# Kernel optimization log

Hardware: AMD Instinct MI355X
Metric: run time of the kernel (lower is better)

The kernel has to match this reference:

```python
import jax, jax.numpy as jnp
import numpy as np

N = 50000
E = 800000
IN_C = 128
HID = 64
HEADS = 4
OUT_C = 1
NEG_SLOPE = 0.2  # PyG GATConv default


def setup_inputs() -> dict:
    key = jax.random.key(0)
    ks = jax.random.split(key, 12)
    s = 1.0 / np.sqrt(IN_C)
    s2 = 1.0 / np.sqrt(HEADS * HID)
    return {
        "x": jax.random.normal(ks[0], (N, IN_C), jnp.float32),
        "edge_index": jax.random.randint(ks[1], (2, E), 0, N, jnp.int64),
        # layer 1 params (heads=HEADS, concat=True)
        "W1": jax.random.normal(ks[2], (IN_C, HEADS * HID), jnp.float32) * s,
        "att_src1": jax.random.normal(ks[3], (HEADS, HID), jnp.float32) * s,
        "att_dst1": jax.random.normal(ks[4], (HEADS, HID), jnp.float32) * s,
        "b1": jnp.zeros((HEADS * HID,), jnp.float32),
        # layer 2 params (heads=1, concat=False)
        "W2": jax.random.normal(ks[5], (HEADS * HID, OUT_C), jnp.float32) * s2,
        "att_src2": jax.random.normal(ks[6], (1, OUT_C), jnp.float32) * s2,
        "att_dst2": jax.random.normal(ks[7], (1, OUT_C), jnp.float32) * s2,
        "b2": jnp.zeros((OUT_C,), jnp.float32),
    }


def _gat_layer(x, src, dst, W, att_src, att_dst, b, concat):
    heads, out_c = att_src.shape
    h = (x @ W).reshape(-1, heads, out_c)          # [N, H, F]
    # per-node attention scores, gathered per edge (scalars, cheap)
    s_src = jnp.einsum('nhf,hf->nh', h, att_src)   # [N, H]
    s_dst = jnp.einsum('nhf,hf->nh', h, att_dst)
    e = jax.nn.leaky_relu(s_src[src] + s_dst[dst], NEG_SLOPE)  # [E, H]
    # segment softmax over edges sharing a destination
    m = jax.ops.segment_max(e, dst, num_segments=N)            # [N, H]
    m = jnp.where(jnp.isfinite(m), m, 0.0)
    ex = jnp.exp(e - m[dst])
    denom = jax.ops.segment_sum(ex, dst, num_segments=N)       # [N, H]
    alpha = ex / denom[dst]                                    # [E, H]
    # weighted scatter-aggregate of source features
    agg = jax.ops.segment_sum(alpha[:, :, None] * h[src], dst, num_segments=N)  # [N, H, F]
    out = agg.reshape(-1, heads * out_c) if concat else agg.mean(axis=1)
    return out + b


def reference(x, edge_index, W1, att_src1, att_dst1, b1, W2, att_src2, att_dst2, b2):
    # PyG GATConv default: add self loops
    loop = jnp.arange(N, dtype=edge_index.dtype)
    src = jnp.concatenate([edge_index[0], loop])
    dst = jnp.concatenate([edge_index[1], loop])
    h = _gat_layer(x, src, dst, W1, att_src1, att_dst1, b1, concat=True)
    h = jax.nn.elu(h)
    return _gat_layer(h, src, dst, W2, att_src2, att_dst2, b2, concat=False)
```

## Files before the change

### kernel.cpp

```cpp
#include <hip/hip_runtime.h>
#include <math.h>

#define NN 50000
#define EE 800000
#define ETOT 850000
#define NEG 0.2f
#define CAP 64
#define NBLK 782
#define NSLC 6250
#define FGRP 256
#define NFB (FGRP * 8)
#define CHK2 1661
#define FITER 7
#define CBLK 3321

typedef unsigned short ushort_t;
typedef __attribute__((ext_vector_type(8))) short bf16x8;
typedef __attribute__((ext_vector_type(4))) float f32x4;

__device__ __forceinline__ unsigned f2bf(float f) {
    unsigned u = __float_as_uint(f);
    return (u + 0x7FFFu + ((u >> 16) & 1u)) >> 16;
}
__device__ __forceinline__ unsigned cvtpk(float lo, float hi) {
    unsigned r;
    asm("v_cvt_pk_bf16_f32 %0, %1, %2" : "=v"(r) : "v"(lo), "v"(hi));
    return r;
}
__device__ __forceinline__ float blo(unsigned u) { return __uint_as_float(u << 16); }
__device__ __forceinline__ float bhi(unsigned u) { return __uint_as_float(u & 0xffff0000u); }

__global__ __launch_bounds__(256) void k_prep(const float* __restrict__ W,
                                              const float* __restrict__ b1,
                                              const float* __restrict__ W2,
                                              const void* ei,
                                              ushort_t* __restrict__ Wf,
                                              float* __restrict__ b1q,
                                              float* __restrict__ W2q,
                                              int* __restrict__ cursor,
                                              ushort_t* __restrict__ dst16,
                                              ushort_t* __restrict__ src16) {
    int bid = blockIdx.x, t = threadIdx.x;
    if (bid < 128) {
        int idx = bid * 256 + t;
        int e = idx & 7, l = (idx >> 3) & 63, ct = (idx >> 9) & 15, kt = idx >> 13;
        int k = kt * 32 + (l >> 4) * 8 + e;
        int col = ct * 16 + (l & 15);
        Wf[idx] = (ushort_t)f2bf(W[k * 256 + col]);
        return;
    }
    if (bid == 128) {
        if (t < 64) {
            int c = t;
            int hl = c >> 1, sub = c & 1, head = c >> 4, lrr = c & 15;
#pragma unroll
            for (int kk = 0; kk < 4; ++kk) {
                b1q[hl * 8 + sub * 4 + kk] = b1[head * 64 + lrr + 16 * kk];
                W2q[hl * 8 + sub * 4 + kk] = W2[head * 64 + lrr + 16 * kk];
            }
        }
        return;
    }
    if (bid < 178) {
        int idx = (bid - 129) * 256 + t;
        if (idx < NN / 4) ((int4*)cursor)[idx] = make_int4(0, 0, 0, 0);
        return;
    }
    int lane = t & 63;
    long long probe = ((const long long*)ei)[lane];
    unsigned long long bad = __ballot(probe < 0 || probe >= NN);
    bool f64 = (bad == 0ull);
    int e = (bid - 178) * 256 + t;
    if (e >= ETOT) return;
    int src, dst;
    if (e < EE) {
        if (f64) {
            src = (int)((const long long*)ei)[e];
            dst = (int)((const long long*)ei)[(long long)EE + e];
        } else {
            src = ((const int*)ei)[e];
            dst = ((const int*)ei)[EE + e];
        }
    } else {
        src = dst = e - EE;
    }
    dst16[e] = (ushort_t)dst;
    src16[e] = (ushort_t)src;
}

__global__ __launch_bounds__(256) void k_main(
    const float* __restrict__ x, const ushort_t* __restrict__ Wf,
    const float* __restrict__ aS, const float* __restrict__ aD,
    const ushort_t* __restrict__ dst16, const ushort_t* __restrict__ src16,
    int* cursor, ushort_t* __restrict__ esrc,
    uint2* __restrict__ h1c, float* __restrict__ sS, float* __restrict__ sD) {
    __shared__ ushort_t xs[64][144];
    int bid = blockIdx.x, t = threadIdx.x;
    if (bid >= NBLK) {
        int s = bid & 7;
        int g = (bid - NBLK) >> 3;
        int lo = s * NSLC;
#pragma unroll
        for (int it = 0; it < FITER; ++it) {
            int c = g + it * FGRP;
            if (c >= CHK2) break;
            int eA = c * 512 + t;
            int eB = eA + 256;
            bool vA = eA < ETOT, vB = eB < ETOT;
            int dstA = 0, dstB = 0;
            if (vA) dstA = dst16[eA];
            if (vB) dstB = dst16[eB];
            if (vA && (unsigned)(dstA - lo) < (unsigned)NSLC) {
                int src = src16[eA];
                int pos = atomicAdd(&cursor[dstA], 1);
                if (pos < CAP) esrc[dstA * CAP + pos] = (ushort_t)src;
            }
            if (vB && (unsigned)(dstB - lo) < (unsigned)NSLC) {
                int src = src16[eB];
                int pos = atomicAdd(&cursor[dstB], 1);
                if (pos < CAP) esrc[dstB * CAP + pos] = (ushort_t)src;
            }
        }
        return;
    }
    int wid = t >> 6, l = t & 63;
    int lg = l >> 4, lr = l & 15;
    int r0 = bid * 64;
    int c0 = wid * 64;
    for (int i = t; i < 1024; i += 256) {
        int row = i >> 4, c = i & 15;
        int gr = r0 + row;
        if (gr >= NN) gr = NN - 1;
        const f32x4* p = (const f32x4*)(x + (size_t)gr * 128 + c * 8);
        f32x4 a = __builtin_nontemporal_load(p);
        f32x4 b = __builtin_nontemporal_load(p + 1);
        uint4 v;
        v.x = cvtpk(a.x, a.y);
        v.y = cvtpk(a.z, a.w);
        v.z = cvtpk(b.x, b.y);
        v.w = cvtpk(b.z, b.w);
        *(uint4*)&xs[row][c * 8] = v;
    }
    __syncthreads();
    const bf16x8* Bv = (const bf16x8*)Wf;
    f32x4 acc[4][4] = {};
#pragma unroll
    for (int kt = 0; kt < 4; ++kt) {
        bf16x8 a[4];
#pragma unroll
        for (int rt = 0; rt < 4; ++rt)
            a[rt] = *(const bf16x8*)&xs[rt * 16 + lr][kt * 32 + lg * 8];
#pragma unroll
        for (int ct = 0; ct < 4; ++ct) {
            bf16x8 b = Bv[(size_t)((kt * 16 + wid * 4 + ct) * 64 + l)];
#pragma unroll
            for (int rt = 0; rt < 4; ++rt)
                acc[rt][ct] = __builtin_amdgcn_mfma_f32_16x16x32_bf16(a[rt], b, acc[rt][ct], 0, 0, 0);
        }
    }
    float aSl[4], aDl[4];
#pragma unroll
    for (int ct = 0; ct < 4; ++ct) {
        aSl[ct] = aS[c0 + ct * 16 + lr];
        aDl[ct] = aD[c0 + ct * 16 + lr];
    }
#pragma unroll
    for (int rt = 0; rt < 4; ++rt) {
#pragma unroll
        for (int q = 0; q < 4; ++q) {
            int row = r0 + rt * 16 + lg * 4 + q;
            bool ok = row < NN;
            float v0 = acc[rt][0][q], v1 = acc[rt][1][q];
            float v2 = acc[rt][2][q], v3 = acc[rt][3][q];
            float p = v0 * aSl[0] + v1 * aSl[1] + v2 * aSl[2] + v3 * aSl[3];
            float dd = v0 * aDl[0] + v1 * aDl[1] + v2 * aDl[2] + v3 * aDl[3];
            uint2 u;
            u.x = cvtpk(v0, v1);
            u.y = cvtpk(v2, v3);
            if (ok) h1c[(size_t)row * 64 + wid * 16 + lr] = u;
#pragma unroll
            for (int k = 8; k >= 1; k >>= 1) {
                p += __shfl_xor(p, k, 64);
                dd += __shfl_xor(dd, k, 64);
            }
            if (ok && lr == 0) {
                sS[row * 4 + wid] = p;
                sD[row * 4 + wid] = dd;
            }
        }
    }
}

__global__ __launch_bounds__(256) void k_agg1(
    const int* __restrict__ cursor, const ushort_t* __restrict__ esrc,
    const uint4* __restrict__ h1c4, const float* __restrict__ sS,
    const float* __restrict__ sD, const float* __restrict__ b1q,
    const float* __restrict__ W2q, float* __restrict__ g) {
    __shared__ float al_lds[4][CAP][4];
    __shared__ int s_lds[4][CAP];
    int wid = threadIdx.x >> 6, lane = threadIdx.x & 63;
    int n = blockIdx.x * 4 + wid;
    if (n >= NN) return;
    int d = cursor[n];
    if (d > CAP) d = CAP;
    int dp = (d + 7) & ~7;
    float4 sd = *(const float4*)(sD + (size_t)n * 4);
    float e0 = -1e30f, e1 = -1e30f, e2 = -1e30f, e3 = -1e30f;
    int s = 0;
    if (lane < d) {
        s = esrc[n * CAP + lane];
        float4 ss = *(const float4*)(sS + (size_t)s * 4);
        e0 = ss.x + sd.x; e0 = e0 > 0.f ? e0 : NEG * e0;
        e1 = ss.y + sd.y; e1 = e1 > 0.f ? e1 : NEG * e1;
        e2 = ss.z + sd.z; e2 = e2 > 0.f ? e2 : NEG * e2;
        e3 = ss.w + sd.w; e3 = e3 > 0.f ? e3 : NEG * e3;
    }
    float m0 = e0, m1 = e1, m2 = e2, m3 = e3;
#pragma unroll
    for (int k = 32; k >= 1; k >>= 1) {
        m0 = fmaxf(m0, __shfl_xor(m0, k, 64));
        m1 = fmaxf(m1, __shfl_xor(m1, k, 64));
        m2 = fmaxf(m2, __shfl_xor(m2, k, 64));
        m3 = fmaxf(m3, __shfl_xor(m3, k, 64));
    }
    float x0 = __expf(e0 - m0);
    float x1 = __expf(e1 - m1);
    float x2 = __expf(e2 - m2);
    float x3 = __expf(e3 - m3);
    float q0 = x0, q1 = x1, q2 = x2, q3 = x3;
#pragma unroll
    for (int k = 32; k >= 1; k >>= 1) {
        q0 += __shfl_xor(q0, k, 64);
        q1 += __shfl_xor(q1, k, 64);
        q2 += __shfl_xor(q2, k, 64);
        q3 += __shfl_xor(q3, k, 64);
    }
    if (lane < dp) {
        al_lds[wid][lane][0] = x0 / q0;
        al_lds[wid][lane][1] = x1 / q1;
        al_lds[wid][lane][2] = x2 / q2;
        al_lds[wid][lane][3] = x3 / q3;
        s_lds[wid][lane] = s;
    }
    __builtin_amdgcn_s_barrier();
    int hl = lane & 31, p = lane >> 5;
    int head = hl >> 3;
    float a0 = 0.f, a1 = 0.f, a2 = 0.f, a3 = 0.f;
    float a4 = 0.f, a5 = 0.f, a6 = 0.f, a7 = 0.f;
    for (int j = 0; j < dp; j += 8) {
        int i0 = j + p, i1 = j + 2 + p, i2 = j + 4 + p, i3 = j + 6 + p;
        int s0 = s_lds[wid][i0];
        int s1 = s_lds[wid][i1];
        int s2 = s_lds[wid][i2];
        int s3 = s_lds[wid][i3];
        float w0 = al_lds[wid][i0][head];
        float w1 = al_lds[wid][i1][head];
        float w2 = al_lds[wid][i2][head];
        float w3 = al_lds[wid][i3][head];
        uint4 u0 = h1c4[(size_t)s0 * 32 + hl];
        uint4 u1 = h1c4[(size_t)s1 * 32 + hl];
        uint4 u2 = h1c4[(size_t)s2 * 32 + hl];
        uint4 u3 = h1c4[(size_t)s3 * 32 + hl];
        a0 = fmaf(w0, blo(u0.x), a0); a1 = fmaf(w0, bhi(u0.x), a1);
        a2 = fmaf(w0, blo(u0.y), a2); a3 = fmaf(w0, bhi(u0.y), a3);
        a4 = fmaf(w0, blo(u0.z), a4); a5 = fmaf(w0, bhi(u0.z), a5);
        a6 = fmaf(w0, blo(u0.w), a6); a7 = fmaf(w0, bhi(u0.w), a7);
        a0 = fmaf(w1, blo(u1.x), a0); a1 = fmaf(w1, bhi(u1.x), a1);
        a2 = fmaf(w1, blo(u1.y), a2); a3 = fmaf(w1, bhi(u1.y), a3);
        a4 = fmaf(w1, blo(u1.z), a4); a5 = fmaf(w1, bhi(u1.z), a5);
        a6 = fmaf(w1, blo(u1.w), a6); a7 = fmaf(w1, bhi(u1.w), a7);
        a0 = fmaf(w2, blo(u2.x), a0); a1 = fmaf(w2, bhi(u2.x), a1);
        a2 = fmaf(w2, blo(u2.y), a2); a3 = fmaf(w2, bhi(u2.y), a3);
        a4 = fmaf(w2, blo(u2.z), a4); a5 = fmaf(w2, bhi(u2.z), a5);
        a6 = fmaf(w2, blo(u2.w), a6); a7 = fmaf(w2, bhi(u2.w), a7);
        a0 = fmaf(w3, blo(u3.x), a0); a1 = fmaf(w3, bhi(u3.x), a1);
        a2 = fmaf(w3, blo(u3.y), a2); a3 = fmaf(w3, bhi(u3.y), a3);
        a4 = fmaf(w3, blo(u3.z), a4); a5 = fmaf(w3, bhi(u3.z), a5);
        a6 = fmaf(w3, blo(u3.w), a6); a7 = fmaf(w3, bhi(u3.w), a7);
    }
    a0 += __shfl_xor(a0, 32, 64); a1 += __shfl_xor(a1, 32, 64);
    a2 += __shfl_xor(a2, 32, 64); a3 += __shfl_xor(a3, 32, 64);
    a4 += __shfl_xor(a4, 32, 64); a5 += __shfl_xor(a5, 32, 64);
    a6 += __shfl_xor(a6, 32, 64); a7 += __shfl_xor(a7, 32, 64);
    float4 bA = ((const float4*)b1q)[hl * 2];
    float4 bB = ((const float4*)b1q)[hl * 2 + 1];
    float4 wA = ((const float4*)W2q)[hl * 2];
    float4 wB = ((const float4*)W2q)[hl * 2 + 1];
    float o0 = a0 + bA.x, o1 = a1 + bA.y, o2 = a2 + bA.z, o3 = a3 + bA.w;
    float o4 = a4 + bB.x, o5 = a5 + bB.y, o6 = a6 + bB.z, o7 = a7 + bB.w;
    o0 = o0 > 0.f ? o0 : expm1f(o0);
    o1 = o1 > 0.f ? o1 : expm1f(o1);
    o2 = o2 > 0.f ? o2 : expm1f(o2);
    o3 = o3 > 0.f ? o3 : expm1f(o3);
    o4 = o4 > 0.f ? o4 : expm1f(o4);
    o5 = o5 > 0.f ? o5 : expm1f(o5);
    o6 = o6 > 0.f ? o6 : expm1f(o6);
    o7 = o7 > 0.f ? o7 : expm1f(o7);
    float part = o0 * wA.x + o1 * wA.y + o2 * wA.z + o3 * wA.w
               + o4 * wB.x + o5 * wB.y + o6 * wB.z + o7 * wB.w;
#pragma unroll
    for (int k = 16; k >= 1; k >>= 1) part += __shfl_xor(part, k, 64);
    if (lane == 0) g[n] = part;
}

__global__ __launch_bounds__(256) void k_layer2(
    const int* __restrict__ cursor, const ushort_t* __restrict__ esrc,
    const float* __restrict__ g, const float* __restrict__ aS2,
    const float* __restrict__ aD2, const float* __restrict__ b2,
    float* __restrict__ out) {
    int wid = threadIdx.x >> 6, lane = threadIdx.x & 63;
    int n = blockIdx.x * 4 + wid;
    if (n >= NN) return;
    int d = cursor[n];
    if (d > CAP) d = CAP;
    float aS = aS2[0], aD = aD2[0];
    float dn = g[n] * aD;
    float gv = 0.f, e = -1e30f;
    if (lane < d) {
        gv = g[esrc[n * CAP + lane]];
        e = gv * aS + dn;
        e = e > 0.f ? e : NEG * e;
    }
    float m = e;
#pragma unroll
    for (int k = 32; k >= 1; k >>= 1) m = fmaxf(m, __shfl_xor(m, k, 64));
    float ex = (lane < d) ? __expf(e - m) : 0.f;
    float den = ex, ws = ex * gv;
#pragma unroll
    for (int k = 32; k >= 1; k >>= 1) {
        den += __shfl_xor(den, k, 64);
        ws += __shfl_xor(ws, k, 64);
    }
    if (lane == 0) out[n] = ws / den + b2[0];
}

extern "C" void kernel_launch(void* const* d_in, const int* in_sizes, int n_in,
                              void* d_out, int out_size, void* d_ws, size_t ws_size,
                              hipStream_t stream) {
    const float* x   = (const float*)d_in[0];
    const void*  ei  = d_in[1];
    const float* W1  = (const float*)d_in[2];
    const float* aS1 = (const float*)d_in[3];
    const float* aD1 = (const float*)d_in[4];
    const float* b1  = (const float*)d_in[5];
    const float* W2  = (const float*)d_in[6];
    const float* aS2 = (const float*)d_in[7];
    const float* aD2 = (const float*)d_in[8];
    const float* b2  = (const float*)d_in[9];
    float* out = (float*)d_out;

    char* w = (char*)d_ws;
    size_t off = 0;
    auto take = [&](size_t bytes) {
        char* p = w + off;
        off = (off + bytes + 255) & ~(size_t)255;
        return p;
    };
    int*      cursor = (int*)take((size_t)NN * 4);
    ushort_t* esrc   = (ushort_t*)take((size_t)NN * CAP * 2);
    ushort_t* dst16  = (ushort_t*)take((size_t)ETOT * 2);
    ushort_t* src16  = (ushort_t*)take((size_t)ETOT * 2);
    float*    sS     = (float*)take((size_t)NN * 4 * 4);
    float*    sD     = (float*)take((size_t)NN * 4 * 4);
    float*    g      = (float*)take((size_t)NN * 4);
    void*     h1c    = take((size_t)NN * 64 * 8);
    ushort_t* Wf     = (ushort_t*)take((size_t)128 * 256 * 2);
    float*    b1q    = (float*)take((size_t)256 * 4);
    float*    W2q    = (float*)take((size_t)256 * 4);
    (void)ws_size; (void)in_sizes; (void)n_in; (void)out_size;

    k_prep<<<178 + CBLK, 256, 0, stream>>>(W1, b1, W2, ei, Wf, b1q, W2q,
                                           cursor, dst16, src16);
    k_main<<<NBLK + NFB, 256, 0, stream>>>(x, Wf, aS1, aD1, dst16, src16,
                                           cursor, esrc, (uint2*)h1c, sS, sD);
    k_agg1<<<12500, 256, 0, stream>>>(cursor, esrc, (const uint4*)h1c, sS, sD, b1q, W2q, g);
    k_layer2<<<12500, 256, 0, stream>>>(cursor, esrc, g, aS2, aD2, b2, out);
}
```

Baseline: 142.8 us.

## Vectorize edge bucketing loads and split layer-1 aggregation into two launches

The bucketing blocks in k_main now load 8 consecutive dst/src indices per thread with 128-bit loads, replacing the strided two-edge-per-iteration loop. FGRP grows so each block covers 2048 edges in a single pass. Separately, k_agg1 takes a base node offset and is launched twice over halves of the nodes, which adds a launch while changing how blocks are scheduled. Atomics per thread are now serialized in 8-element runs, which may lower memory-level parallelism.

```diff
diff --git a/kernel.cpp b/kernel.cpp
--- a/kernel.cpp
+++ b/kernel.cpp
@@ -8,10 +8,8 @@
 #define CAP 64
 #define NBLK 782
 #define NSLC 6250
-#define FGRP 256
+#define FGRP 416
 #define NFB (FGRP * 8)
-#define CHK2 1661
-#define FITER 7
 #define CBLK 3321
 
 typedef unsigned short ushort_t;
@@ -98,27 +96,36 @@
     int bid = blockIdx.x, t = threadIdx.x;
     if (bid >= NBLK) {
         int s = bid & 7;
-        int g = (bid - NBLK) >> 3;
+        int grp = (bid - NBLK) >> 3;
         int lo = s * NSLC;
-#pragma unroll
-        for (int it = 0; it < FITER; ++it) {
-            int c = g + it * FGRP;
-            if (c >= CHK2) break;
-            int eA = c * 512 + t;
-            int eB = eA + 256;
-            bool vA = eA < ETOT, vB = eB < ETOT;
-            int dstA = 0, dstB = 0;
-            if (vA) dstA = dst16[eA];
-            if (vB) dstB = dst16[eB];
-            if (vA && (unsigned)(dstA - lo) < (unsigned)NSLC) {
-                int src = src16[eA];
-                int pos = atomicAdd(&cursor[dstA], 1);
-                if (pos < CAP) esrc[dstA * CAP + pos] = (ushort_t)src;
-            }
-            if (vB && (unsigned)(dstB - lo) < (unsigned)NSLC) {
-                int src = src16[eB];
-                int pos = atomicAdd(&cursor[dstB], 1);
-                if (pos < CAP) esrc[dstB * CAP + pos] = (ushort_t)src;
+        int e0 = grp * 2048 + t * 8;
+        if (e0 >= ETOT) return;
+        ushort_t d[8], sv[8];
+        if (e0 + 8 <= ETOT) {
+            uint4 dv = *(const uint4*)(dst16 + e0);
+            uint4 vv = *(const uint4*)(src16 + e0);
+            d[0] = (ushort_t)dv.x; d[1] = (ushort_t)(dv.x >> 16);
+            d[2] = (ushort_t)dv.y; d[3] = (ushort_t)(dv.y >> 16);
+            d[4] = (ushort_t)dv.z; d[5] = (ushort_t)(dv.z >> 16);
+            d[6] = (ushort_t)dv.w; d[7] = (ushort_t)(dv.w >> 16);
+            sv[0] = (ushort_t)vv.x; sv[1] = (ushort_t)(vv.x >> 16);
+            sv[2] = (ushort_t)vv.y; sv[3] = (ushort_t)(vv.y >> 16);
+            sv[4] = (ushort_t)vv.z; sv[5] = (ushort_t)(vv.z >> 16);
+            sv[6] = (ushort_t)vv.w; sv[7] = (ushort_t)(vv.w >> 16);
+#pragma unroll
+            for (int k = 0; k < 8; ++k) {
+                if ((unsigned)(d[k] - lo) < (unsigned)NSLC) {
+                    int pos = atomicAdd(&cursor[d[k]], 1);
+                    if (pos < CAP) esrc[d[k] * CAP + pos] = sv[k];
+                }
+            }
+        } else {
+            for (int k = 0; k < 8 && e0 + k < ETOT; ++k) {
+                int dd = dst16[e0 + k];
+                if ((unsigned)(dd - lo) < (unsigned)NSLC) {
+                    int pos = atomicAdd(&cursor[dd], 1);
+                    if (pos < CAP) esrc[dd * CAP + pos] = src16[e0 + k];
+                }
             }
         }
         return;
@@ -195,11 +202,11 @@
     const int* __restrict__ cursor, const ushort_t* __restrict__ esrc,
     const uint4* __restrict__ h1c4, const float* __restrict__ sS,
     const float* __restrict__ sD, const float* __restrict__ b1q,
-    const float* __restrict__ W2q, float* __restrict__ g) {
+    const float* __restrict__ W2q, float* __restrict__ g, int base) {
     __shared__ float al_lds[4][CAP][4];
     __shared__ int s_lds[4][CAP];
     int wid = threadIdx.x >> 6, lane = threadIdx.x & 63;
-    int n = blockIdx.x * 4 + wid;
+    int n = base + blockIdx.x * 4 + wid;
     if (n >= NN) return;
     int d = cursor[n];
     if (d > CAP) d = CAP;
@@ -373,6 +380,7 @@
                                            cursor, dst16, src16);
     k_main<<<NBLK + NFB, 256, 0, stream>>>(x, Wf, aS1, aD1, dst16, src16,
                                            cursor, esrc, (uint2*)h1c, sS, sD);
-    k_agg1<<<12500, 256, 0, stream>>>(cursor, esrc, (const uint4*)h1c, sS, sD, b1q, W2q, g);
+    k_agg1<<<6250, 256, 0, stream>>>(cursor, esrc, (const uint4*)h1c, sS, sD, b1q, W2q, g, 0);
+    k_agg1<<<6250, 256, 0, stream>>>(cursor, esrc, (const uint4*)h1c, sS, sD, b1q, W2q, g, 25000);
     k_layer2<<<12500, 256, 0, stream>>>(cursor, esrc, g, aS2, aD2, b2, out);
 }
```

After: 146.9 us. 2.9% more time.
